# Kernel tuning notes

Hardware: AMD Instinct MI355X
Metric: run time of the kernel (lower is better)

Reference implementation:

```python
import jax, jax.numpy as jnp
import numpy as np


def _conv3d(x, w, pad, groups=1):
    # x: [N,C,D,H,W]; w: [O,I/groups,kd,kh,kw]; cross-correlation, same as torch conv3d
    return jax.lax.conv_general_dilated(
        x, w, window_strides=(1, 1, 1),
        padding=[(p, p) for p in pad],
        dimension_numbers=('NCDHW', 'OIDHW', 'NCDHW'),
        feature_group_count=groups)


def setup_inputs() -> dict:
    key = jax.random.key(0)
    D = 192
    x = jax.random.normal(key, (1, 1, D, D, D), dtype=jnp.float32)

    # Gaussian kernel: sigma=1.0 -> radius=3 -> 7^3
    sigma = 1.0
    radius = int(3 * sigma)
    c = jnp.arange(-radius, radius + 1, dtype=jnp.float32)
    g1 = jnp.exp(-c ** 2 / (2.0 * sigma * sigma))
    g1 = g1 / g1.sum()
    g3 = g1[:, None, None] * g1[None, :, None] * g1[None, None, :]
    gauss3d = g3[None, None]  # [1,1,7,7,7]

    # Pavel derivative kernels (outer products of d [len 9] and s [len 5])
    d = jnp.array([2.0, 1.0, -16.0, -27.0, 0.0, 27.0, 16.0, -1.0, -2.0], dtype=jnp.float32)
    s = jnp.array([1.0, 4.0, 6.0, 4.0, 1.0], dtype=jnp.float32)
    norm = 96.0 * 16.0 * 16.0
    kz = (d[:, None, None] * s[None, :, None] * s[None, None, :] / norm)[None, None]  # [1,1,9,5,5]
    ky = (s[:, None, None] * d[None, :, None] * s[None, None, :] / norm)[None, None]  # [1,1,5,9,5]
    kx = (s[:, None, None] * s[None, :, None] * d[None, None, :] / norm)[None, None]  # [1,1,5,5,9]

    return {"x": x, "gauss3d": gauss3d, "kz": kz, "ky": ky, "kx": kx}


def reference(x, gauss3d, kz, ky, kx):
    pad = (gauss3d.shape[2] - 1) // 2  # radius = 3
    # sigma > 0: pre-smooth input
    xs = _conv3d(x, gauss3d, (pad, pad, pad))
    # gradient components
    gz = _conv3d(xs, kz, (4, 2, 2))
    gy = _conv3d(xs, ky, (2, 4, 2))
    gx = _conv3d(xs, kx, (2, 2, 4))
    # structure-tensor components, channel order [Jzz, Jzy, Jzx, Jyy, Jyx, Jxx]
    J = jnp.concatenate([gz * gz, gy * gz, gx * gz, gy * gy, gx * gy, gx * gx], axis=1)
    # smooth_components=True: grouped Gaussian smoothing of each component
    g6 = jnp.broadcast_to(gauss3d, (6,) + gauss3d.shape[1:])  # [6,1,7,7,7]
    J = _conv3d(J, g6, (pad, pad, pad), groups=6)
    return J
```

## Files before the change

### kernel.cpp

```cpp
#include <hip/hip_runtime.h>


constexpr int D  = 192;
constexpr int DD = D * D;
constexpr long long V = (long long)D * DD;

__global__ void setup_coef(const float* __restrict__ g3, const float* __restrict__ kz,
                           const float* __restrict__ ky, const float* __restrict__ kx,
                           float* __restrict__ c) {
    if (blockIdx.x != 0 || threadIdx.x != 0) return;
    float Tg = g3[0];
    for (int i = 0; i < 7; ++i) c[0 + i]  = g3[i * 49];
    for (int j = 0; j < 7; ++j) c[7 + j]  = g3[j * 7] / Tg;
    for (int k = 0; k < 7; ++k) c[14 + k] = g3[k] / Tg;
    float Tz = kz[0];
    for (int i = 0; i < 9; ++i) c[21 + i] = kz[i * 25];
    for (int j = 0; j < 5; ++j) c[30 + j] = kz[j * 5] / Tz;
    for (int k = 0; k < 5; ++k) c[35 + k] = kz[k] / Tz;
    float Ty = ky[0];
    for (int i = 0; i < 5; ++i) c[40 + i] = ky[i * 45];
    for (int j = 0; j < 9; ++j) c[45 + j] = ky[j * 5] / Ty;
    for (int k = 0; k < 5; ++k) c[54 + k] = ky[k] / Ty;
    float Tx = kx[0];
    for (int i = 0; i < 5; ++i) c[59 + i] = kx[i * 45];
    for (int j = 0; j < 5; ++j) c[64 + j] = kx[j * 9] / Tx;
    for (int k = 0; k < 9; ++k) c[69 + k] = kx[k] / Tx;
}

__device__ inline void load_slice41(const float* __restrict__ src, float* __restrict__ dst,
                                    int rows, int y0, int x0) {
    const int nq = rows * 10;
    for (int li = threadIdx.x; li < nq; li += 256) {
        const int r = li / 10, q = li % 10;
        const int gy = y0 + r, gx = x0 + q * 4;
        float4 v = {0.f, 0.f, 0.f, 0.f};
        if (gy >= 0 && gy < D) {
            if (gx >= 0 && gx + 3 < D) {
                v = *(const float4*)(src + gy * D + gx);
            } else {
                float* pv = (float*)&v;
                for (int j = 0; j < 4; ++j) {
                    const int g = gx + j;
                    if (g >= 0 && g < D) pv[j] = src[gy * D + g];
                }
            }
        }
        float* d = &dst[r * 41 + q * 4];
        d[0] = v.x; d[1] = v.y; d[2] = v.z; d[3] = v.w;
    }
}

template <int SEG, int NCH>
__global__ __launch_bounds__(256) void blur3d(const float* __restrict__ in,
                                              float* __restrict__ out,
                                              const float* __restrict__ coef) {
    __shared__ float raw[38 * 41];
    __shared__ float xt[38][32];
    const int cpx = gridDim.x >> 3;
    int w = (blockIdx.x & 7) * cpx + (blockIdx.x >> 3);
    const int tile = w % 36; w /= 36;
    const int ch = w % NCH;
    const int seg = w / NCH;
    const int tx0 = (tile % 6) * 32, ty0 = (tile / 6) * 32;
    const int z0 = seg * SEG;
    const float* src = in + (long long)ch * V;
    float* dst = out + (long long)ch * V;
    float ga[7], gb[7], gc[7];
#pragma unroll
    for (int k = 0; k < 7; ++k) { ga[k] = coef[k]; gb[k] = coef[7 + k]; gc[k] = coef[14 + k]; }
    const int rr = threadIdx.x >> 3;
    const int cc = (threadIdx.x & 7) * 4;
    float4 ring[7];
#pragma unroll
    for (int k = 0; k < 7; ++k) ring[k] = make_float4(0.f, 0.f, 0.f, 0.f);

    for (int s = z0 - 3; s < z0 + SEG + 3; ++s) {
        const bool inz = (s >= 0 && s < D);
        if (inz) load_slice41(src + (long long)s * DD, raw, 38, ty0 - 3, tx0 - 4);
        __syncthreads();
        if (inz) {
            for (int li = threadIdx.x; li < 38 * 8; li += 256) {
                const int r = li >> 3, g = li & 7;
                const float* rp = &raw[r * 41 + 4 * g + 1];
                float win[10];
#pragma unroll
                for (int i = 0; i < 10; ++i) win[i] = rp[i];
                float4 o = make_float4(0.f, 0.f, 0.f, 0.f);
#pragma unroll
                for (int k = 0; k < 7; ++k) {
                    o.x += gc[k] * win[k];
                    o.y += gc[k] * win[k + 1];
                    o.z += gc[k] * win[k + 2];
                    o.w += gc[k] * win[k + 3];
                }
                *(float4*)&xt[r][4 * g] = o;
            }
        }
        __syncthreads();
        float4 yv = make_float4(0.f, 0.f, 0.f, 0.f);
        if (inz) {
#pragma unroll
            for (int k = 0; k < 7; ++k) {
                const float4 v = *(const float4*)&xt[rr + k][cc];
                yv.x += gb[k] * v.x; yv.y += gb[k] * v.y;
                yv.z += gb[k] * v.z; yv.w += gb[k] * v.w;
            }
        }
#pragma unroll
        for (int k = 0; k < 6; ++k) ring[k] = ring[k + 1];
        ring[6] = yv;
        const int z = s - 3;
        if (z >= z0) {
            float4 a = make_float4(0.f, 0.f, 0.f, 0.f);
#pragma unroll
            for (int k = 0; k < 7; ++k) {
                a.x += ga[k] * ring[k].x; a.y += ga[k] * ring[k].y;
                a.z += ga[k] * ring[k].z; a.w += ga[k] * ring[k].w;
            }
            *(float4*)(dst + (long long)z * DD + (ty0 + rr) * D + tx0 + cc) = a;
        }
    }
}

template <int SEG>
__global__ __launch_bounds__(256) void gradprod3d(const float* __restrict__ xs,
                                                  float* __restrict__ P,
                                                  const float* __restrict__ coef) {
    __shared__ float raw[24 * 41];
    __shared__ float X1[24][32];
    __shared__ float X2[24][32];
    const int cpx = gridDim.x >> 3;
    int w = (blockIdx.x & 7) * cpx + (blockIdx.x >> 3);
    const int tile = w % 72;
    const int seg = w / 72;
    const int tx0 = (tile % 6) * 32, ty0 = (tile / 6) * 16;
    const int z0 = seg * SEG;
    float az[9], ay[5], ax[5], bz[5], by[9], bx[5], czc[5], cxc[9];
#pragma unroll
    for (int k = 0; k < 9; ++k) az[k] = coef[21 + k];
#pragma unroll
    for (int k = 0; k < 5; ++k) ay[k] = coef[40 + k];
#pragma unroll
    for (int k = 0; k < 5; ++k) ax[k] = coef[59 + k];
#pragma unroll
    for (int k = 0; k < 5; ++k) bz[k] = coef[30 + k];
#pragma unroll
    for (int k = 0; k < 9; ++k) by[k] = coef[45 + k];
#pragma unroll
    for (int k = 0; k < 5; ++k) bx[k] = coef[64 + k];
#pragma unroll
    for (int k = 0; k < 5; ++k) czc[k] = coef[35 + k];
#pragma unroll
    for (int k = 0; k < 9; ++k) cxc[k] = coef[69 + k];
    const int rr = threadIdx.x >> 4;
    const int cc = (threadIdx.x & 15) * 2;
    float2 R1[9], R2[7], R3[7];
#pragma unroll
    for (int k = 0; k < 9; ++k) R1[k] = make_float2(0.f, 0.f);
#pragma unroll
    for (int k = 0; k < 7; ++k) { R2[k] = make_float2(0.f, 0.f); R3[k] = make_float2(0.f, 0.f); }

    for (int s = z0 - 4; s < z0 + SEG + 4; ++s) {
        const bool inz = (s >= 0 && s < D);
        if (inz) load_slice41(xs + (long long)s * DD, raw, 24, ty0 - 4, tx0 - 4);
        __syncthreads();
        if (inz && threadIdx.x < 192) {
            const int r = threadIdx.x >> 3, g = threadIdx.x & 7;
            const float* rp = &raw[r * 41 + 4 * g];
            float win[12];
#pragma unroll
            for (int i = 0; i < 12; ++i) win[i] = rp[i];
            float4 o1 = make_float4(0.f, 0.f, 0.f, 0.f);
            float4 o2 = make_float4(0.f, 0.f, 0.f, 0.f);
#pragma unroll
            for (int k = 0; k < 5; ++k) {
                o1.x += czc[k] * win[2 + k];
                o1.y += czc[k] * win[3 + k];
                o1.z += czc[k] * win[4 + k];
                o1.w += czc[k] * win[5 + k];
            }
#pragma unroll
            for (int k = 0; k < 9; ++k) {
                o2.x += cxc[k] * win[k];
                o2.y += cxc[k] * win[1 + k];
                o2.z += cxc[k] * win[2 + k];
                o2.w += cxc[k] * win[3 + k];
            }
            *(float4*)&X1[r][4 * g] = o1;
            *(float4*)&X2[r][4 * g] = o2;
        }
        __syncthreads();
        float2 t1 = make_float2(0.f, 0.f), t2 = t1, t3 = t1;
        if (inz) {
#pragma unroll
            for (int k = 0; k < 5; ++k) {
                const float2 v = *(const float2*)&X1[rr + 2 + k][cc];
                t1.x += bz[k] * v.x; t1.y += bz[k] * v.y;
            }
#pragma unroll
            for (int k = 0; k < 9; ++k) {
                const float2 v = *(const float2*)&X1[rr + k][cc];
                t2.x += by[k] * v.x; t2.y += by[k] * v.y;
            }
#pragma unroll
            for (int k = 0; k < 5; ++k) {
                const float2 v = *(const float2*)&X2[rr + 2 + k][cc];
                t3.x += bx[k] * v.x; t3.y += bx[k] * v.y;
            }
        }
#pragma unroll
        for (int k = 0; k < 8; ++k) R1[k] = R1[k + 1];
        R1[8] = t1;
#pragma unroll
        for (int k = 0; k < 6; ++k) { R2[k] = R2[k + 1]; R3[k] = R3[k + 1]; }
        R2[6] = t2; R3[6] = t3;
        const int z = s - 4;
        if (z >= z0) {
            float gz0 = 0.f, gz1 = 0.f, gy0 = 0.f, gy1 = 0.f, gx0 = 0.f, gx1 = 0.f;
#pragma unroll
            for (int k = 0; k < 9; ++k) { gz0 += az[k] * R1[k].x; gz1 += az[k] * R1[k].y; }
#pragma unroll
            for (int k = 0; k < 5; ++k) {
                gy0 += ay[k] * R2[k].x; gy1 += ay[k] * R2[k].y;
                gx0 += ax[k] * R3[k].x; gx1 += ax[k] * R3[k].y;
            }
            float* o = P + (long long)z * DD + (ty0 + rr) * D + tx0 + cc;
            float2 wv;
            wv.x = gz0 * gz0; wv.y = gz1 * gz1; *(float2*)(o + 0 * V) = wv;
            wv.x = gy0 * gz0; wv.y = gy1 * gz1; *(float2*)(o + 1 * V) = wv;
            wv.x = gx0 * gz0; wv.y = gx1 * gz1; *(float2*)(o + 2 * V) = wv;
            wv.x = gy0 * gy0; wv.y = gy1 * gy1; *(float2*)(o + 3 * V) = wv;
            wv.x = gx0 * gy0; wv.y = gx1 * gy1; *(float2*)(o + 4 * V) = wv;
            wv.x = gx0 * gx0; wv.y = gx1 * gx1; *(float2*)(o + 5 * V) = wv;
        }
    }
}

extern "C" void kernel_launch(void* const* d_in, const int* in_sizes, int n_in,
                              void* d_out, int out_size, void* d_ws, size_t ws_size,
                              hipStream_t stream) {
    const float* x  = (const float*)d_in[0];
    const float* g3 = (const float*)d_in[1];
    const float* kz = (const float*)d_in[2];
    const float* ky = (const float*)d_in[3];
    const float* kx = (const float*)d_in[4];
    float* out = (float*)d_out;

    float* coef = (float*)d_ws;
    float* P  = coef + 128;
    float* xs = P + 6 * V;

    setup_coef<<<1, 64, 0, stream>>>(g3, kz, ky, kx, coef);

    blur3d<6, 1><<<1152, 256, 0, stream>>>(x, xs, coef);

    gradprod3d<12><<<1152, 256, 0, stream>>>(xs, P, coef);

    blur3d<24, 6><<<1728, 256, 0, stream>>>(P, out, coef);
}
```

Before: 177.8 us.

## Prefetch next z-slice into registers to overlap global loads with compute

Both the blur and gradient kernels now issue the global loads for slice s+1 into registers right after the barrier, then store them to shared memory at the start of the next iteration. This register double-buffering lets the load latency hide behind the per-slice stencil compute instead of stalling before each barrier. The load loop is also unrolled into fixed per-thread tasks. The cost is extra registers held live across the compute phase, which may lower occupancy.

```diff
diff --git a/kernel.cpp b/kernel.cpp
--- a/kernel.cpp
+++ b/kernel.cpp
@@ -27,27 +27,32 @@
     for (int k = 0; k < 9; ++k) c[69 + k] = kx[k] / Tx;
 }
 
-__device__ inline void load_slice41(const float* __restrict__ src, float* __restrict__ dst,
-                                    int rows, int y0, int x0) {
-    const int nq = rows * 10;
-    for (int li = threadIdx.x; li < nq; li += 256) {
-        const int r = li / 10, q = li % 10;
-        const int gy = y0 + r, gx = x0 + q * 4;
-        float4 v = {0.f, 0.f, 0.f, 0.f};
-        if (gy >= 0 && gy < D) {
-            if (gx >= 0 && gx + 3 < D) {
-                v = *(const float4*)(src + gy * D + gx);
-            } else {
-                float* pv = (float*)&v;
-                for (int j = 0; j < 4; ++j) {
-                    const int g = gx + j;
-                    if (g >= 0 && g < D) pv[j] = src[gy * D + g];
-                }
-            }
-        }
-        float* d = &dst[r * 41 + q * 4];
-        d[0] = v.x; d[1] = v.y; d[2] = v.z; d[3] = v.w;
-    }
+__device__ inline float4 ldg4(const float* __restrict__ slice, int gy, int gx) {
+    float4 v = {0.f, 0.f, 0.f, 0.f};
+    if ((unsigned)gy < (unsigned)D) {
+        const float* row = slice + gy * D;
+        if ((unsigned)gx <= (unsigned)(D - 4)) {
+            v = *(const float4*)(row + gx);
+        } else {
+            float* pv = (float*)&v;
+#pragma unroll
+            for (int j = 0; j < 4; ++j) {
+                const int g = gx + j;
+                if ((unsigned)g < (unsigned)D) pv[j] = row[g];
+            }
+        }
+    }
+    return v;
+}
+
+__device__ inline float4 ld_task10(const float* __restrict__ slice, int y0, int x0, int li) {
+    const int r = li / 10, q = li % 10;
+    return ldg4(slice, y0 + r, x0 + q * 4);
+}
+__device__ inline void st_task41(float* __restrict__ dst, int li, float4 v) {
+    const int r = li / 10, q = li % 10;
+    float* d = &dst[r * 41 + q * 4];
+    d[0] = v.x; d[1] = v.y; d[2] = v.z; d[3] = v.w;
 }
 
 template <int SEG, int NCH>
@@ -68,18 +73,36 @@
     float ga[7], gb[7], gc[7];
 #pragma unroll
     for (int k = 0; k < 7; ++k) { ga[k] = coef[k]; gb[k] = coef[7 + k]; gc[k] = coef[14 + k]; }
-    const int rr = threadIdx.x >> 3;
-    const int cc = (threadIdx.x & 7) * 4;
+    const int tid = threadIdx.x;
+    const int rr = tid >> 3;
+    const int cc = (tid & 7) * 4;
+    const bool t2 = tid < 38 * 10 - 256;
     float4 ring[7];
 #pragma unroll
     for (int k = 0; k < 7; ++k) ring[k] = make_float4(0.f, 0.f, 0.f, 0.f);
+
+    float4 p0 = make_float4(0.f, 0.f, 0.f, 0.f), p1 = p0;
+    if (z0 - 3 >= 0) {
+        const float* sl = src + (long long)(z0 - 3) * DD;
+        p0 = ld_task10(sl, ty0 - 3, tx0 - 4, tid);
+        if (t2) p1 = ld_task10(sl, ty0 - 3, tx0 - 4, tid + 256);
+    }
 
     for (int s = z0 - 3; s < z0 + SEG + 3; ++s) {
         const bool inz = (s >= 0 && s < D);
-        if (inz) load_slice41(src + (long long)s * DD, raw, 38, ty0 - 3, tx0 - 4);
-        __syncthreads();
-        if (inz) {
-            for (int li = threadIdx.x; li < 38 * 8; li += 256) {
+        if (inz) {
+            st_task41(raw, tid, p0);
+            if (t2) st_task41(raw, tid + 256, p1);
+        }
+        __syncthreads();
+        const int sn = s + 1;
+        if (sn < z0 + SEG + 3 && sn >= 0 && sn < D) {
+            const float* sl = src + (long long)sn * DD;
+            p0 = ld_task10(sl, ty0 - 3, tx0 - 4, tid);
+            if (t2) p1 = ld_task10(sl, ty0 - 3, tx0 - 4, tid + 256);
+        }
+        if (inz) {
+            for (int li = tid; li < 38 * 8; li += 256) {
                 const int r = li >> 3, g = li & 7;
                 const float* rp = &raw[r * 41 + 4 * g + 1];
                 float win[10];
@@ -152,20 +175,29 @@
     for (int k = 0; k < 5; ++k) czc[k] = coef[35 + k];
 #pragma unroll
     for (int k = 0; k < 9; ++k) cxc[k] = coef[69 + k];
-    const int rr = threadIdx.x >> 4;
-    const int cc = (threadIdx.x & 15) * 2;
+    const int tid = threadIdx.x;
+    const int rr = tid >> 4;
+    const int cc = (tid & 15) * 2;
+    const bool hast = tid < 240;
     float2 R1[9], R2[7], R3[7];
 #pragma unroll
     for (int k = 0; k < 9; ++k) R1[k] = make_float2(0.f, 0.f);
 #pragma unroll
     for (int k = 0; k < 7; ++k) { R2[k] = make_float2(0.f, 0.f); R3[k] = make_float2(0.f, 0.f); }
+
+    float4 p0 = make_float4(0.f, 0.f, 0.f, 0.f);
+    if (z0 - 4 >= 0 && hast)
+        p0 = ld_task10(xs + (long long)(z0 - 4) * DD, ty0 - 4, tx0 - 4, tid);
 
     for (int s = z0 - 4; s < z0 + SEG + 4; ++s) {
         const bool inz = (s >= 0 && s < D);
-        if (inz) load_slice41(xs + (long long)s * DD, raw, 24, ty0 - 4, tx0 - 4);
-        __syncthreads();
-        if (inz && threadIdx.x < 192) {
-            const int r = threadIdx.x >> 3, g = threadIdx.x & 7;
+        if (inz && hast) st_task41(raw, tid, p0);
+        __syncthreads();
+        const int sn = s + 1;
+        if (sn < z0 + SEG + 4 && sn >= 0 && sn < D && hast)
+            p0 = ld_task10(xs + (long long)sn * DD, ty0 - 4, tx0 - 4, tid);
+        if (inz && tid < 192) {
+            const int r = tid >> 3, g = tid & 7;
             const float* rp = &raw[r * 41 + 4 * g];
             float win[12];
 #pragma unroll
```

New measurement: 209.2 us. 1.18x slower.

## Store gradients only and fuse structure-tensor products into final blur load

Applied to the files above, without the earlier changes.

The gradient kernel now writes three gradient volumes instead of six product volumes. The final grouped Gaussian blur computes each tensor component on the fly by loading one or two gradient slices and multiplying them before staging into shared memory. This halves the intermediate write traffic and workspace. In exchange the off-diagonal channels read two input volumes per slice, so read traffic in the last pass rises.

```diff
diff --git a/kernel.cpp b/kernel.cpp
--- a/kernel.cpp
+++ b/kernel.cpp
@@ -27,30 +27,35 @@
     for (int k = 0; k < 9; ++k) c[69 + k] = kx[k] / Tx;
 }
 
-__device__ inline void load_slice41(const float* __restrict__ src, float* __restrict__ dst,
-                                    int rows, int y0, int x0) {
-    const int nq = rows * 10;
-    for (int li = threadIdx.x; li < nq; li += 256) {
-        const int r = li / 10, q = li % 10;
-        const int gy = y0 + r, gx = x0 + q * 4;
-        float4 v = {0.f, 0.f, 0.f, 0.f};
-        if (gy >= 0 && gy < D) {
-            if (gx >= 0 && gx + 3 < D) {
-                v = *(const float4*)(src + gy * D + gx);
-            } else {
-                float* pv = (float*)&v;
-                for (int j = 0; j < 4; ++j) {
-                    const int g = gx + j;
-                    if (g >= 0 && g < D) pv[j] = src[gy * D + g];
-                }
-            }
-        }
-        float* d = &dst[r * 41 + q * 4];
-        d[0] = v.x; d[1] = v.y; d[2] = v.z; d[3] = v.w;
+__device__ inline float4 ldg4(const float* __restrict__ slice, int gy, int gx) {
+    float4 v = {0.f, 0.f, 0.f, 0.f};
+    if ((unsigned)gy < (unsigned)D) {
+        const float* row = slice + gy * D;
+        if ((unsigned)gx <= (unsigned)(D - 4)) {
+            v = *(const float4*)(row + gx);
+        } else {
+            float* pv = (float*)&v;
+#pragma unroll
+            for (int j = 0; j < 4; ++j) {
+                const int g = gx + j;
+                if ((unsigned)g < (unsigned)D) pv[j] = row[g];
+            }
+        }
     }
-}
-
-template <int SEG, int NCH>
+    return v;
+}
+
+__device__ inline float4 ld_task10(const float* __restrict__ slice, int y0, int x0, int li) {
+    const int r = li / 10, q = li % 10;
+    return ldg4(slice, y0 + r, x0 + q * 4);
+}
+__device__ inline void st_task41(float* __restrict__ dst, int li, float4 v) {
+    const int r = li / 10, q = li % 10;
+    float* d = &dst[r * 41 + q * 4];
+    d[0] = v.x; d[1] = v.y; d[2] = v.z; d[3] = v.w;
+}
+
+template <int SEG, int NCH, bool PROD>
 __global__ __launch_bounds__(256) void blur3d(const float* __restrict__ in,
                                               float* __restrict__ out,
                                               const float* __restrict__ coef) {
@@ -63,7 +68,11 @@
     const int seg = w / NCH;
     const int tx0 = (tile % 6) * 32, ty0 = (tile / 6) * 32;
     const int z0 = seg * SEG;
-    const float* src = in + (long long)ch * V;
+    const int IA[6] = {0, 1, 2, 1, 2, 2};
+    const int IB[6] = {0, 0, 0, 1, 1, 2};
+    const float* srcA = in + (long long)(PROD ? IA[ch] : ch) * V;
+    const float* srcB = in + (long long)(PROD ? IB[ch] : ch) * V;
+    const bool same = !PROD || (IA[ch] == IB[ch]);
     float* dst = out + (long long)ch * V;
     float ga[7], gb[7], gc[7];
 #pragma unroll
@@ -76,7 +85,24 @@
 
     for (int s = z0 - 3; s < z0 + SEG + 3; ++s) {
         const bool inz = (s >= 0 && s < D);
-        if (inz) load_slice41(src + (long long)s * DD, raw, 38, ty0 - 3, tx0 - 4);
+        if (inz) {
+            const float* slA = srcA + (long long)s * DD;
+            const float* slB = srcB + (long long)s * DD;
+            if (same) {
+                for (int li = threadIdx.x; li < 380; li += 256) {
+                    float4 a = ld_task10(slA, ty0 - 3, tx0 - 4, li);
+                    if (PROD) { a.x *= a.x; a.y *= a.y; a.z *= a.z; a.w *= a.w; }
+                    st_task41(raw, li, a);
+                }
+            } else {
+                for (int li = threadIdx.x; li < 380; li += 256) {
+                    float4 a = ld_task10(slA, ty0 - 3, tx0 - 4, li);
+                    float4 b = ld_task10(slB, ty0 - 3, tx0 - 4, li);
+                    a.x *= b.x; a.y *= b.y; a.z *= b.z; a.w *= b.w;
+                    st_task41(raw, li, a);
+                }
+            }
+        }
         __syncthreads();
         if (inz) {
             for (int li = threadIdx.x; li < 38 * 8; li += 256) {
@@ -123,9 +149,9 @@
 }
 
 template <int SEG>
-__global__ __launch_bounds__(256) void gradprod3d(const float* __restrict__ xs,
-                                                  float* __restrict__ P,
-                                                  const float* __restrict__ coef) {
+__global__ __launch_bounds__(256) void grad3d(const float* __restrict__ xs,
+                                              float* __restrict__ G,
+                                              const float* __restrict__ coef) {
     __shared__ float raw[24 * 41];
     __shared__ float X1[24][32];
     __shared__ float X2[24][32];
@@ -162,7 +188,11 @@
 
     for (int s = z0 - 4; s < z0 + SEG + 4; ++s) {
         const bool inz = (s >= 0 && s < D);
-        if (inz) load_slice41(xs + (long long)s * DD, raw, 24, ty0 - 4, tx0 - 4);
+        if (inz) {
+            const float* sl = xs + (long long)s * DD;
+            for (int li = threadIdx.x; li < 240; li += 256)
+                st_task41(raw, li, ld_task10(sl, ty0 - 4, tx0 - 4, li));
+        }
         __syncthreads();
         if (inz && threadIdx.x < 192) {
             const int r = threadIdx.x >> 3, g = threadIdx.x & 7;
@@ -224,14 +254,11 @@
                 gy0 += ay[k] * R2[k].x; gy1 += ay[k] * R2[k].y;
                 gx0 += ax[k] * R3[k].x; gx1 += ax[k] * R3[k].y;
             }
-            float* o = P + (long long)z * DD + (ty0 + rr) * D + tx0 + cc;
+            float* o = G + (long long)z * DD + (ty0 + rr) * D + tx0 + cc;
             float2 wv;
-            wv.x = gz0 * gz0; wv.y = gz1 * gz1; *(float2*)(o + 0 * V) = wv;
-            wv.x = gy0 * gz0; wv.y = gy1 * gz1; *(float2*)(o + 1 * V) = wv;
-            wv.x = gx0 * gz0; wv.y = gx1 * gz1; *(float2*)(o + 2 * V) = wv;
-            wv.x = gy0 * gy0; wv.y = gy1 * gy1; *(float2*)(o + 3 * V) = wv;
-            wv.x = gx0 * gy0; wv.y = gx1 * gy1; *(float2*)(o + 4 * V) = wv;
-            wv.x = gx0 * gx0; wv.y = gx1 * gx1; *(float2*)(o + 5 * V) = wv;
+            wv.x = gz0; wv.y = gz1; *(float2*)(o + 0 * V) = wv;
+            wv.x = gy0; wv.y = gy1; *(float2*)(o + 1 * V) = wv;
+            wv.x = gx0; wv.y = gx1; *(float2*)(o + 2 * V) = wv;
         }
     }
 }
@@ -247,14 +274,14 @@
     float* out = (float*)d_out;
 
     float* coef = (float*)d_ws;
-    float* P  = coef + 128;
-    float* xs = P + 6 * V;
+    float* G  = coef + 128;
+    float* xs = G + 3 * V;
 
     setup_coef<<<1, 64, 0, stream>>>(g3, kz, ky, kx, coef);
 
-    blur3d<6, 1><<<1152, 256, 0, stream>>>(x, xs, coef);
-
-    gradprod3d<12><<<1152, 256, 0, stream>>>(xs, P, coef);
-
-    blur3d<24, 6><<<1728, 256, 0, stream>>>(P, out, coef);
-}
+    blur3d<6, 1, false><<<1152, 256, 0, stream>>>(x, xs, coef);
+
+    grad3d<12><<<1152, 256, 0, stream>>>(xs, G, coef);
+
+    blur3d<24, 6, true><<<1728, 256, 0, stream>>>(G, out, coef);
+}
```

After: 168.6 us. 5.1% less time.
